# Performance work log

Measured on AMD Instinct MI355X. Metric: run time of the kernel, lower is better.

## Reference

```python
import jax, jax.numpy as jnp
import numpy as np

IN_CH, D, K = 256, 128, 512

def setup_inputs() -> dict:
    key = jax.random.key(0)
    k1, k2, k3, k4 = jax.random.split(key, 4)
    x = jax.random.normal(k1, (16, IN_CH, 64, 64), dtype=jnp.float32)
    W = jax.random.normal(k2, (D, IN_CH), dtype=jnp.float32) * (1.0 / np.sqrt(IN_CH))
    b = jax.random.normal(k3, (D,), dtype=jnp.float32) * 0.01
    prototypes = jax.random.normal(k4, (K, D), dtype=jnp.float32) * 0.02
    gamma = jnp.asarray(1.0, dtype=jnp.float32)
    return {"x": x, "W": W, "b": b, "prototypes": prototypes, "gamma": gamma}

def reference(x, W, b, prototypes, gamma):
    n, c, h, w = x.shape
    # 1x1 conv projection: [n,c,h,w] -> [n,h,w,d]
    q = jnp.einsum('nchw,dc->nhwd', x, W) + b
    q_flat = q.reshape(n * h * w, -1)                      # [T, d]
    q_norm2 = jnp.sum(q_flat * q_flat, axis=1, keepdims=True)   # [T, 1]
    p_norm2 = jnp.sum(prototypes * prototypes, axis=1)[None, :] # [1, K]
    dist2 = q_norm2 + p_norm2 - 2.0 * (q_flat @ prototypes.T)   # [T, K]
    weights = jax.nn.softmax(-jnp.abs(gamma) * dist2, axis=1)
    return weights.reshape(n, h, w, -1).transpose(0, 3, 1, 2)   # [n, K, h, w]
```

## Files before the change

kernel.cpp:

```cpp
#include <hip/hip_runtime.h>

#define HW 4096
#define NCH 256
#define DIM 128
#define NPROTO 512

typedef __attribute__((ext_vector_type(4))) float f32x4;
typedef __attribute__((ext_vector_type(8))) short s16x8;

__device__ __forceinline__ unsigned short f2bf(float f) {
  union { float f; unsigned u; } v; v.f = f;
  unsigned r = v.u + 0x7fffu + ((v.u >> 16) & 1u);
  return (unsigned short)(r >> 16);
}

__device__ __forceinline__ void gload_lds16(const void* g, void* l) {
  __builtin_amdgcn_global_load_lds(
      (const __attribute__((address_space(1))) void*)g,
      (__attribute__((address_space(3))) void*)l, 16, 0, 0);
}

__global__ __launch_bounds__(256) void prep_kernel(const float* __restrict__ P,
                                                   const float* __restrict__ Wm,
                                                   unsigned short* __restrict__ Pr,
                                                   unsigned short* __restrict__ Wbf,
                                                   float* __restrict__ pn2) {
  const int tid = threadIdx.x;
  const int b = blockIdx.x;
  if (b < 8) {
    const int n  = b * 64 + (tid >> 2);
    const int qt = tid & 3;
    const float* row = P + n * DIM + qt * 32;
    unsigned short* dst = Pr + ((size_t)qt * NPROTO + n) * 32;
    float ssq = 0.f;
#pragma unroll
    for (int u = 0; u < 8; ++u) {
      f32x4 v = *(const f32x4*)(row + 4 * u);
      ssq += v.x * v.x + v.y * v.y + v.z * v.z + v.w * v.w;
      dst[4 * u + 0] = f2bf(v.x);
      dst[4 * u + 1] = f2bf(v.y);
      dst[4 * u + 2] = f2bf(v.z);
      dst[4 * u + 3] = f2bf(v.w);
    }
    ssq += __shfl_xor(ssq, 1);
    ssq += __shfl_xor(ssq, 2);
    if (qt == 0) pn2[n] = ssq;
  } else {
    const int idx = ((b - 8) * 256 + tid) * 16;
#pragma unroll
    for (int u = 0; u < 4; ++u) {
      f32x4 v = *(const f32x4*)(Wm + idx + 4 * u);
      unsigned short* d = Wbf + idx + 4 * u;
      d[0] = f2bf(v.x); d[1] = f2bf(v.y); d[2] = f2bf(v.z); d[3] = f2bf(v.w);
    }
  }
}

__global__ __launch_bounds__(512, 4) void fused_kernel(
    const float* __restrict__ x, const unsigned short* __restrict__ Wbf,
    const float* __restrict__ bias, const unsigned short* __restrict__ Pr,
    const float* __restrict__ pn2, const float* __restrict__ gptr,
    float* __restrict__ out) {
  __shared__ __align__(16) char smem[70144];
  unsigned short* q_s = (unsigned short*)smem;
  char* x_b = smem + 16384;
  char* wsb = smem + 16384 + 18432;
  char* P_w = smem + 16384;
  float* red  = (float*)(smem + 67584);
  float* rmx  = (float*)(smem + 69632);
  float* rinv = (float*)(smem + 69888);

  const int tid  = threadIdx.x;
  const int p0   = blockIdx.x * 64;
  const int nimg = p0 >> 12;
  const int hw0  = p0 & 4095;
  const int wave = tid >> 6, lane = tid & 63;
  const int l15 = lane & 15, l4 = lane >> 4;
  const int wr = wave >> 2, wc = wave & 3;

  f32x4 acc1[2][2];
#pragma unroll
  for (int i = 0; i < 2; ++i)
#pragma unroll
    for (int j = 0; j < 2; ++j)
#pragma unroll
      for (int r = 0; r < 4; ++r) acc1[i][j][r] = 0.f;

  const float* xb = x + (size_t)nimg * NCH * HW + hw0;
  const int f  = tid & 15;
  const int cp = tid >> 4;
  const int wrow = 8 * wave + (lane >> 3);
  const int wu   = lane & 7;

#pragma unroll
  for (int t = 0; t < 2; ++t) {
    const int row = 64 * t + wrow;
    gload_lds16(Wbf + (size_t)row * NCH + ((wu ^ (row & 7)) << 3),
                wsb + t * 8192 + wave * 1024);
  }
  f32x4 cv0 = *(const f32x4*)(xb + (size_t)(2 * cp + 0) * HW + 4 * f);
  f32x4 cv1 = *(const f32x4*)(xb + (size_t)(2 * cp + 1) * HW + 4 * f);

#pragma unroll
  for (int it = 0; it < 4; ++it) {
    const int buf = it & 1;
    const int c0n = 64 * (it + 1);
    if (it < 3) {
#pragma unroll
      for (int t = 0; t < 2; ++t) {
        const int row = 64 * t + wrow;
        gload_lds16(Wbf + (size_t)row * NCH + c0n + ((wu ^ (row & 7)) << 3),
                    wsb + (buf ^ 1) * 16384 + t * 8192 + wave * 1024);
      }
    }
    f32x4 nv0 = cv0, nv1 = cv1;
    if (it < 3) {
      nv0 = *(const f32x4*)(xb + (size_t)(c0n + 2 * cp + 0) * HW + 4 * f);
      nv1 = *(const f32x4*)(xb + (size_t)(c0n + 2 * cp + 1) * HW + 4 * f);
    }
#pragma unroll
    for (int s = 0; s < 4; ++s) {
      const int row = 4 * f + s;
      unsigned pk = (unsigned)f2bf(cv0[s]) | ((unsigned)f2bf(cv1[s]) << 16);
      *(unsigned*)(x_b + buf * 9216 + row * 144 +
                   ((4 * cp) ^ (((row >> 2) & 7) << 4))) = pk;
    }
    if (it < 3) asm volatile("s_waitcnt vmcnt(4) lgkmcnt(0)" ::: "memory");
    else        asm volatile("s_waitcnt vmcnt(0) lgkmcnt(0)" ::: "memory");
    __builtin_amdgcn_s_barrier();
#pragma unroll
    for (int kc = 0; kc < 64; kc += 32) {
      const int ub = (kc >> 3) + l4;
      s16x8 a[2];
#pragma unroll
      for (int i = 0; i < 2; ++i) {
        const int row = 32 * wr + 16 * i + l15;
        a[i] = *(const s16x8*)(x_b + buf * 9216 + row * 144 +
                               16 * (ub ^ ((row >> 2) & 7)));
      }
#pragma unroll
      for (int j = 0; j < 2; ++j) {
        s16x8 b = *(const s16x8*)(wsb + buf * 16384 +
                                  (32 * wc + 16 * j + l15) * 128 +
                                  ((ub ^ (l15 & 7)) << 4));
#pragma unroll
        for (int i = 0; i < 2; ++i)
          acc1[i][j] = __builtin_amdgcn_mfma_f32_16x16x32_bf16(a[i], b, acc1[i][j], 0, 0, 0);
      }
    }
    asm volatile("s_waitcnt lgkmcnt(0)" ::: "memory");
    __builtin_amdgcn_s_barrier();
    cv0 = nv0; cv1 = nv1;
  }

#pragma unroll
  for (int t = 0; t < 4; ++t)
    gload_lds16(Pr + (size_t)(64 * wave + 16 * t) * 32 + 8 * lane,
                P_w + wave * 4096 + t * 1024);

#pragma unroll
  for (int j = 0; j < 2; ++j) {
    const int d = 32 * wc + 16 * j + l15;
    const float bv = bias[d];
    const int u  = d >> 3;
    const int d7 = d & 7;
#pragma unroll
    for (int i = 0; i < 2; ++i) {
      const int pxb = 32 * wr + 16 * i + 4 * l4;
#pragma unroll
      for (int r = 0; r < 4; ++r) {
        const int px = pxb + r;
        q_s[px * 128 + ((u ^ (px & 7)) << 3) + d7] = f2bf(acc1[i][j][r] + bv);
      }
    }
  }
  __syncthreads();

  f32x4 acc[4][4];
#pragma unroll
  for (int i = 0; i < 4; ++i)
#pragma unroll
    for (int j = 0; j < 4; ++j)
#pragma unroll
      for (int r = 0; r < 4; ++r) acc[i][j][r] = 0.f;

  const unsigned short* Pw = (const unsigned short*)(P_w + wave * 4096);

#pragma unroll
  for (int ch = 0; ch < 4; ++ch) {
    if (ch) asm volatile("s_waitcnt vmcnt(0)" ::: "memory");
    s16x8 afr[4];
#pragma unroll
    for (int i = 0; i < 4; ++i) {
      const int px = 16 * i + l15;
      afr[i] = *(const s16x8*)&q_s[px * 128 + (((4 * ch + l4) ^ (l15 & 7)) << 3)];
    }
#pragma unroll
    for (int j = 0; j < 4; ++j) {
      s16x8 bfr = *(const s16x8*)&Pw[(16 * j + l15) * 32 + 8 * l4];
#pragma unroll
      for (int i = 0; i < 4; ++i)
        acc[i][j] = __builtin_amdgcn_mfma_f32_16x16x32_bf16(afr[i], bfr, acc[i][j], 0, 0, 0);
    }
    if (ch < 3) {
      __builtin_amdgcn_sched_barrier(0);
#pragma unroll
      for (int t = 0; t < 4; ++t)
        gload_lds16(Pr + (size_t)((ch + 1) * NPROTO + 64 * wave + 16 * t) * 32 + 8 * lane,
                    P_w + wave * 4096 + t * 1024);
    }
  }

  const float g2  = fabsf(gptr[0]) * 1.44269504088896340736f;
  const float tg2 = 2.f * g2;
  float cj[4];
#pragma unroll
  for (int j = 0; j < 4; ++j) cj[j] = g2 * pn2[64 * wave + 16 * j + l15];

#pragma unroll
  for (int i = 0; i < 4; ++i)
#pragma unroll
    for (int r = 0; r < 4; ++r) {
      float m = -1e30f;
#pragma unroll
      for (int j = 0; j < 4; ++j) {
        float lv = fmaf(acc[i][j][r], tg2, -cj[j]);
        acc[i][j][r] = lv;
        m = fmaxf(m, lv);
      }
#pragma unroll
      for (int s = 1; s < 16; s <<= 1) m = fmaxf(m, __shfl_xor(m, s));
      if (l15 == 0) red[wave * 64 + 16 * i + 4 * l4 + r] = m;
    }
  __syncthreads();
  if (tid < 64) {
    float M = red[tid];
#pragma unroll
    for (int w = 1; w < 8; ++w) M = fmaxf(M, red[w * 64 + tid]);
    rmx[tid] = M;
  }
  __syncthreads();

#pragma unroll
  for (int i = 0; i < 4; ++i) {
    const f32x4 Mi = *(const f32x4*)&rmx[16 * i + 4 * l4];
#pragma unroll
    for (int r = 0; r < 4; ++r) {
      float s = 0.f;
#pragma unroll
      for (int j = 0; j < 4; ++j) {
        float e = exp2f(acc[i][j][r] - Mi[r]);
        acc[i][j][r] = e;
        s += e;
      }
#pragma unroll
      for (int t = 1; t < 16; t <<= 1) s += __shfl_xor(s, t);
      if (l15 == 0) red[wave * 64 + 16 * i + 4 * l4 + r] = s;
    }
  }
  __syncthreads();
  if (tid < 64) {
    float S = 0.f;
#pragma unroll
    for (int w = 0; w < 8; ++w) S += red[w * 64 + tid];
    rinv[tid] = 1.f / S;
  }
  __syncthreads();

  float* ob = out + (size_t)nimg * NPROTO * HW + hw0;
#pragma unroll
  for (int i = 0; i < 4; ++i) {
    const f32x4 iv = *(const f32x4*)&rinv[16 * i + 4 * l4];
    const int px = 16 * i + 4 * l4;
#pragma unroll
    for (int j = 0; j < 4; ++j) {
      const int k = 64 * wave + 16 * j + l15;
      f32x4 o = acc[i][j] * iv;
      *(f32x4*)(ob + (size_t)k * HW + px) = o;
    }
  }
}

extern "C" void kernel_launch(void* const* d_in, const int* in_sizes, int n_in,
                              void* d_out, int out_size, void* d_ws, size_t ws_size,
                              hipStream_t stream) {
  const float* x     = (const float*)d_in[0];
  const float* Wm    = (const float*)d_in[1];
  const float* bias  = (const float*)d_in[2];
  const float* prot  = (const float*)d_in[3];
  const float* gamma = (const float*)d_in[4];
  float* out = (float*)d_out;

  unsigned short* Pr_w  = (unsigned short*)d_ws;
  float*          pn2_w = (float*)((char*)d_ws + 131072);
  unsigned short* W_ws  = (unsigned short*)((char*)d_ws + 131072 + 2048);

  prep_kernel<<<16, 256, 0, stream>>>(prot, Wm, Pr_w, W_ws, pn2_w);
  fused_kernel<<<1024, 512, 0, stream>>>(x, W_ws, bias, Pr_w, pn2_w, gamma, out);
}
```

Baseline: 213.8 us.

## Halve pixel tile per block, single-buffer W, load prototypes directly to registers

```diff
diff --git a/kernel.cpp b/kernel.cpp
--- a/kernel.cpp
+++ b/kernel.cpp
@@ -56,39 +56,36 @@
   }
 }
 
-__global__ __launch_bounds__(512, 4) void fused_kernel(
+__global__ __launch_bounds__(512, 6) void fused_kernel(
     const float* __restrict__ x, const unsigned short* __restrict__ Wbf,
     const float* __restrict__ bias, const unsigned short* __restrict__ Pr,
     const float* __restrict__ pn2, const float* __restrict__ gptr,
     float* __restrict__ out) {
-  __shared__ __align__(16) char smem[70144];
+  __shared__ __align__(16) char smem[35072];
   unsigned short* q_s = (unsigned short*)smem;
-  char* x_b = smem + 16384;
-  char* wsb = smem + 16384 + 18432;
-  char* P_w = smem + 16384;
-  float* red  = (float*)(smem + 67584);
-  float* rmx  = (float*)(smem + 69632);
-  float* rinv = (float*)(smem + 69888);
+  char* x_b = smem + 8192;
+  char* wsb = smem + 17408;
+  float* red  = (float*)(smem + 33792);
+  float* rmx  = (float*)(smem + 34816);
+  float* rinv = (float*)(smem + 34944);
 
   const int tid  = threadIdx.x;
-  const int p0   = blockIdx.x * 64;
+  const int p0   = blockIdx.x * 32;
   const int nimg = p0 >> 12;
   const int hw0  = p0 & 4095;
   const int wave = tid >> 6, lane = tid & 63;
   const int l15 = lane & 15, l4 = lane >> 4;
   const int wr = wave >> 2, wc = wave & 3;
 
-  f32x4 acc1[2][2];
-#pragma unroll
-  for (int i = 0; i < 2; ++i)
-#pragma unroll
-    for (int j = 0; j < 2; ++j)
-#pragma unroll
-      for (int r = 0; r < 4; ++r) acc1[i][j][r] = 0.f;
+  f32x4 acc1[2];
+#pragma unroll
+  for (int j = 0; j < 2; ++j)
+#pragma unroll
+    for (int r = 0; r < 4; ++r) acc1[j][r] = 0.f;
 
   const float* xb = x + (size_t)nimg * NCH * HW + hw0;
-  const int f  = tid & 15;
-  const int cp = tid >> 4;
+  const int f  = tid & 7;
+  const int cp = tid >> 3;
   const int wrow = 8 * wave + (lane >> 3);
   const int wu   = lane & 7;
 
@@ -98,65 +95,61 @@
     gload_lds16(Wbf + (size_t)row * NCH + ((wu ^ (row & 7)) << 3),
                 wsb + t * 8192 + wave * 1024);
   }
-  f32x4 cv0 = *(const f32x4*)(xb + (size_t)(2 * cp + 0) * HW + 4 * f);
-  f32x4 cv1 = *(const f32x4*)(xb + (size_t)(2 * cp + 1) * HW + 4 * f);
+  f32x4 cv0 = {0,0,0,0}, cv1 = {0,0,0,0};
+  if (tid < 256) {
+    cv0 = *(const f32x4*)(xb + (size_t)(2 * cp + 0) * HW + 4 * f);
+    cv1 = *(const f32x4*)(xb + (size_t)(2 * cp + 1) * HW + 4 * f);
+  }
 
 #pragma unroll
   for (int it = 0; it < 4; ++it) {
     const int buf = it & 1;
     const int c0n = 64 * (it + 1);
+    f32x4 nv0 = cv0, nv1 = cv1;
+    if (tid < 256) {
+#pragma unroll
+      for (int s = 0; s < 4; ++s) {
+        const int row = 4 * f + s;
+        unsigned pk = (unsigned)f2bf(cv0[s]) | ((unsigned)f2bf(cv1[s]) << 16);
+        *(unsigned*)(x_b + buf * 4608 + row * 144 +
+                     ((4 * cp) ^ (((row >> 2) & 7) << 4))) = pk;
+      }
+      if (it < 3) {
+        nv0 = *(const f32x4*)(xb + (size_t)(c0n + 2 * cp + 0) * HW + 4 * f);
+        nv1 = *(const f32x4*)(xb + (size_t)(c0n + 2 * cp + 1) * HW + 4 * f);
+        asm volatile("s_waitcnt vmcnt(2) lgkmcnt(0)" ::: "memory");
+      } else {
+        asm volatile("s_waitcnt vmcnt(0) lgkmcnt(0)" ::: "memory");
+      }
+    } else {
+      asm volatile("s_waitcnt vmcnt(0)" ::: "memory");
+    }
+    __builtin_amdgcn_s_barrier();
+#pragma unroll
+    for (int kc = 0; kc < 64; kc += 32) {
+      const int ub = (kc >> 3) + l4;
+      const int row = 16 * wr + l15;
+      s16x8 a = *(const s16x8*)(x_b + buf * 4608 + row * 144 +
+                                16 * (ub ^ ((row >> 2) & 7)));
+#pragma unroll
+      for (int j = 0; j < 2; ++j) {
+        s16x8 b = *(const s16x8*)(wsb + (32 * wc + 16 * j + l15) * 128 +
+                                  ((ub ^ (l15 & 7)) << 4));
+        acc1[j] = __builtin_amdgcn_mfma_f32_16x16x32_bf16(a, b, acc1[j], 0, 0, 0);
+      }
+    }
+    asm volatile("s_waitcnt lgkmcnt(0)" ::: "memory");
+    __builtin_amdgcn_s_barrier();
     if (it < 3) {
 #pragma unroll
       for (int t = 0; t < 2; ++t) {
         const int row = 64 * t + wrow;
         gload_lds16(Wbf + (size_t)row * NCH + c0n + ((wu ^ (row & 7)) << 3),
-                    wsb + (buf ^ 1) * 16384 + t * 8192 + wave * 1024);
-      }
-    }
-    f32x4 nv0 = cv0, nv1 = cv1;
-    if (it < 3) {
-      nv0 = *(const f32x4*)(xb + (size_t)(c0n + 2 * cp + 0) * HW + 4 * f);
-      nv1 = *(const f32x4*)(xb + (size_t)(c0n + 2 * cp + 1) * HW + 4 * f);
-    }
-#pragma unroll
-    for (int s = 0; s < 4; ++s) {
-      const int row = 4 * f + s;
-      unsigned pk = (unsigned)f2bf(cv0[s]) | ((unsigned)f2bf(cv1[s]) << 16);
-      *(unsigned*)(x_b + buf * 9216 + row * 144 +
-                   ((4 * cp) ^ (((row >> 2) & 7) << 4))) = pk;
-    }
-    if (it < 3) asm volatile("s_waitcnt vmcnt(4) lgkmcnt(0)" ::: "memory");
-    else        asm volatile("s_waitcnt vmcnt(0) lgkmcnt(0)" ::: "memory");
-    __builtin_amdgcn_s_barrier();
-#pragma unroll
-    for (int kc = 0; kc < 64; kc += 32) {
-      const int ub = (kc >> 3) + l4;
-      s16x8 a[2];
-#pragma unroll
-      for (int i = 0; i < 2; ++i) {
-        const int row = 32 * wr + 16 * i + l15;
-        a[i] = *(const s16x8*)(x_b + buf * 9216 + row * 144 +
-                               16 * (ub ^ ((row >> 2) & 7)));
-      }
-#pragma unroll
-      for (int j = 0; j < 2; ++j) {
-        s16x8 b = *(const s16x8*)(wsb + buf * 16384 +
-                                  (32 * wc + 16 * j + l15) * 128 +
-                                  ((ub ^ (l15 & 7)) << 4));
-#pragma unroll
-        for (int i = 0; i < 2; ++i)
-          acc1[i][j] = __builtin_amdgcn_mfma_f32_16x16x32_bf16(a[i], b, acc1[i][j], 0, 0, 0);
-      }
-    }
-    asm volatile("s_waitcnt lgkmcnt(0)" ::: "memory");
-    __builtin_amdgcn_s_barrier();
+                    wsb + t * 8192 + wave * 1024);
+      }
+    }
     cv0 = nv0; cv1 = nv1;
   }
-
-#pragma unroll
-  for (int t = 0; t < 4; ++t)
-    gload_lds16(Pr + (size_t)(64 * wave + 16 * t) * 32 + 8 * lane,
-                P_w + wave * 4096 + t * 1024);
 
 #pragma unroll
   for (int j = 0; j < 2; ++j) {
@@ -164,50 +157,46 @@
     const float bv = bias[d];
     const int u  = d >> 3;
     const int d7 = d & 7;
+    const int pxb = 16 * wr + 4 * l4;
+#pragma unroll
+    for (int r = 0; r < 4; ++r) {
+      const int px = pxb + r;
+      q_s[px * 128 + ((u ^ (px & 7)) << 3) + d7] = f2bf(acc1[j][r] + bv);
+    }
+  }
+
+  f32x4 acc[2][4];
+#pragma unroll
+  for (int i = 0; i < 2; ++i)
+#pragma unroll
+    for (int j = 0; j < 4; ++j)
+#pragma unroll
+      for (int r = 0; r < 4; ++r) acc[i][j][r] = 0.f;
+
+  s16x8 bq[4];
+#pragma unroll
+  for (int j = 0; j < 4; ++j)
+    bq[j] = *(const s16x8*)(Pr + (size_t)(64 * wave + 16 * j + l15) * 32 + 8 * l4);
+  __syncthreads();
+
+#pragma unroll
+  for (int ch = 0; ch < 4; ++ch) {
+    s16x8 afr[2];
 #pragma unroll
     for (int i = 0; i < 2; ++i) {
-      const int pxb = 32 * wr + 16 * i + 4 * l4;
-#pragma unroll
-      for (int r = 0; r < 4; ++r) {
-        const int px = pxb + r;
-        q_s[px * 128 + ((u ^ (px & 7)) << 3) + d7] = f2bf(acc1[i][j][r] + bv);
-      }
-    }
-  }
-  __syncthreads();
-
-  f32x4 acc[4][4];
-#pragma unroll
-  for (int i = 0; i < 4; ++i)
+      const int px = 16 * i + l15;
+      afr[i] = *(const s16x8*)&q_s[px * 128 + (((4 * ch + l4) ^ (px & 7)) << 3)];
+    }
 #pragma unroll
     for (int j = 0; j < 4; ++j)
 #pragma unroll
-      for (int r = 0; r < 4; ++r) acc[i][j][r] = 0.f;
-
-  const unsigned short* Pw = (const unsigned short*)(P_w + wave * 4096);
-
-#pragma unroll
-  for (int ch = 0; ch < 4; ++ch) {
-    if (ch) asm volatile("s_waitcnt vmcnt(0)" ::: "memory");
-    s16x8 afr[4];
-#pragma unroll
-    for (int i = 0; i < 4; ++i) {
-      const int px = 16 * i + l15;
-      afr[i] = *(const s16x8*)&q_s[px * 128 + (((4 * ch + l4) ^ (l15 & 7)) << 3)];
-    }
-#pragma unroll
-    for (int j = 0; j < 4; ++j) {
-      s16x8 bfr = *(const s16x8*)&Pw[(16 * j + l15) * 32 + 8 * l4];
-#pragma unroll
-      for (int i = 0; i < 4; ++i)
-        acc[i][j] = __builtin_amdgcn_mfma_f32_16x16x32_bf16(afr[i], bfr, acc[i][j], 0, 0, 0);
-    }
+      for (int i = 0; i < 2; ++i)
+        acc[i][j] = __builtin_amdgcn_mfma_f32_16x16x32_bf16(afr[i], bq[j], acc[i][j], 0, 0, 0);
     if (ch < 3) {
       __builtin_amdgcn_sched_barrier(0);
 #pragma unroll
-      for (int t = 0; t < 4; ++t)
-        gload_lds16(Pr + (size_t)((ch + 1) * NPROTO + 64 * wave + 16 * t) * 32 + 8 * lane,
-                    P_w + wave * 4096 + t * 1024);
+      for (int j = 0; j < 4; ++j)
+        bq[j] = *(const s16x8*)(Pr + (size_t)((ch + 1) * NPROTO + 64 * wave + 16 * j + l15) * 32 + 8 * l4);
     }
   }
 
@@ -218,7 +207,7 @@
   for (int j = 0; j < 4; ++j) cj[j] = g2 * pn2[64 * wave + 16 * j + l15];
 
 #pragma unroll
-  for (int i = 0; i < 4; ++i)
+  for (int i = 0; i < 2; ++i)
 #pragma unroll
     for (int r = 0; r < 4; ++r) {
       float m = -1e30f;
@@ -230,19 +219,19 @@
       }
 #pragma unroll
       for (int s = 1; s < 16; s <<= 1) m = fmaxf(m, __shfl_xor(m, s));
-      if (l15 == 0) red[wave * 64 + 16 * i + 4 * l4 + r] = m;
-    }
-  __syncthreads();
-  if (tid < 64) {
+      if (l15 == 0) red[wave * 32 + 16 * i + 4 * l4 + r] = m;
+    }
+  __syncthreads();
+  if (tid < 32) {
     float M = red[tid];
 #pragma unroll
-    for (int w = 1; w < 8; ++w) M = fmaxf(M, red[w * 64 + tid]);
+    for (int w = 1; w < 8; ++w) M = fmaxf(M, red[w * 32 + tid]);
     rmx[tid] = M;
   }
   __syncthreads();
 
 #pragma unroll
-  for (int i = 0; i < 4; ++i) {
+  for (int i = 0; i < 2; ++i) {
     const f32x4 Mi = *(const f32x4*)&rmx[16 * i + 4 * l4];
 #pragma unroll
     for (int r = 0; r < 4; ++r) {
@@ -255,21 +244,21 @@
       }
 #pragma unroll
       for (int t = 1; t < 16; t <<= 1) s += __shfl_xor(s, t);
-      if (l15 == 0) red[wave * 64 + 16 * i + 4 * l4 + r] = s;
-    }
-  }
-  __syncthreads();
-  if (tid < 64) {
+      if (l15 == 0) red[wave * 32 + 16 * i + 4 * l4 + r] = s;
+    }
+  }
+  __syncthreads();
+  if (tid < 32) {
     float S = 0.f;
 #pragma unroll
-    for (int w = 0; w < 8; ++w) S += red[w * 64 + tid];
+    for (int w = 0; w < 8; ++w) S += red[w * 32 + tid];
     rinv[tid] = 1.f / S;
   }
   __syncthreads();
 
   float* ob = out + (size_t)nimg * NPROTO * HW + hw0;
 #pragma unroll
-  for (int i = 0; i < 4; ++i) {
+  for (int i = 0; i < 2; ++i) {
     const f32x4 iv = *(const f32x4*)&rinv[16 * i + 4 * l4];
     const int px = 16 * i + 4 * l4;
 #pragma unroll
@@ -296,5 +285,5 @@
   unsigned short* W_ws  = (unsigned short*)((char*)d_ws + 131072 + 2048);
 
   prep_kernel<<<16, 256, 0, stream>>>(prot, Wm, Pr_w, W_ws, pn2_w);
-  fused_kernel<<<1024, 512, 0, stream>>>(x, W_ws, bias, Pr_w, pn2_w, gamma, out);
-}
+  fused_kernel<<<2048, 512, 0, stream>>>(x, W_ws, bias, Pr_w, pn2_w, gamma, out);
+}
```

Result: slower. 218.7 us (+2.3%).
